# Kernel optimization log

Hardware: AMD Instinct MI355X
Metric: run time of the kernel (lower is better)

The kernel has to match this reference:

```python
import jax, jax.numpy as jnp
import numpy as np

B, D, H, L = 8, 512, 512, 8192


def _log_g(x):
    # log_g(x) = log(relu(x)+1) if x>=0 else x
    return jnp.where(x >= 0, jnp.log1p(jax.nn.relu(x)), x)


def setup_inputs() -> dict:
    key = jax.random.key(0)
    k1, k2, k3 = jax.random.split(key, 3)
    x = jax.random.normal(k1, (B, D, L), dtype=jnp.float32)
    # Conv1d(dim, 2*h_dim, kernel_size=1) weight [2H, D, 1] squeezed to [2H, D]
    W = jax.random.normal(k2, (2 * H, D), dtype=jnp.float32) / np.sqrt(D).astype(np.float32)
    b = jax.random.normal(k3, (2 * H,), dtype=jnp.float32) * 0.02
    return {"x": x, "W": W, "b": b}


def reference(x, W, b):
    # 1x1 conv == pointwise linear over channels: [B, 2H, L]
    hg = jnp.einsum('od,bdl->bol', W, x) + b[None, :, None]
    h, gate = jnp.split(hg, 2, axis=1)  # each [B, H, L]
    log_coeffs = -jax.nn.softplus(gate)                 # log(1 - sigmoid(gate))
    log_values = -jax.nn.softplus(-gate) + _log_g(h)    # log(sigmoid(gate)) + log_g(h)
    a_star = jnp.cumsum(log_coeffs, axis=2)
    log_h = a_star + jax.lax.cumlogsumexp(log_values - a_star, axis=2)
    return jnp.exp(log_h)  # [B, H, L]
```

## Files before the change

kernel.cpp:

```cpp
#include <hip/hip_runtime.h>
#include <hip/hip_fp16.h>

#define B_  8
#define D_  512
#define H_  512
#define L_  8192
#define O2_ 1024

typedef __attribute__((ext_vector_type(8))) short   bf16x8;
typedef __attribute__((ext_vector_type(4))) float   floatx4;
typedef __attribute__((ext_vector_type(8))) unsigned short ushort8_t;
typedef __attribute__((ext_vector_type(4))) unsigned short ushort4_t;

__device__ __forceinline__ unsigned short f2bf(float f) {
    union { float f; unsigned u; } x; x.f = f;
    unsigned u = x.u;
    u += 0x7FFFu + ((u >> 16) & 1u);
    return (unsigned short)(u >> 16);
}

__device__ __forceinline__ void async_load16(const void* g, void* l) {
    __builtin_amdgcn_global_load_lds(
        (const __attribute__((address_space(1))) unsigned int*)g,
        (__attribute__((address_space(3))) unsigned int*)l,
        16, 0, 0);
}

__global__ __launch_bounds__(256) void prep_w(const float* __restrict__ W,
                                              unsigned short* __restrict__ Wr) {
    int idx  = blockIdx.x * 256 + threadIdx.x;
    int flat = idx * 4;
    int o = flat >> 9;
    int d = flat & 511;
    int src_o = (o & 1) ? (H_ + (o >> 1)) : (o >> 1);
    float4 wv = *(const float4*)(W + (size_t)src_o * D_ + d);
    ushort4_t r;
    r.x = f2bf(wv.x); r.y = f2bf(wv.y); r.z = f2bf(wv.z); r.w = f2bf(wv.w);
    *(ushort4_t*)(Wr + (size_t)o * D_ + d) = r;
}

__global__ __launch_bounds__(256) void transpose_x(const float* __restrict__ x,
                                                   unsigned short* __restrict__ xT) {
    __shared__ float T[64][65];
    const int b  = blockIdx.z;
    const int d0 = blockIdx.y * 64;
    const int l0 = blockIdx.x * 64;
    const int tid = threadIdx.x;

    const int c  = tid & 15;
    const int r0 = tid >> 4;
    const float* xp = x + ((size_t)b * D_ + d0) * L_ + l0;
    for (int rr = r0; rr < 64; rr += 16) {
        float4 vv = *(const float4*)(xp + (size_t)rr * L_ + c * 4);
        T[c * 4 + 0][rr] = vv.x;
        T[c * 4 + 1][rr] = vv.y;
        T[c * 4 + 2][rr] = vv.z;
        T[c * 4 + 3][rr] = vv.w;
    }
    __syncthreads();

    const int dc  = (tid & 7) * 8;
    const int lr0 = tid >> 3;
    unsigned short* op = xT + ((size_t)b * L_ + l0) * D_ + d0;
    for (int lr = lr0; lr < 64; lr += 32) {
        ushort8_t o8;
        o8[0] = f2bf(T[lr][dc + 0]); o8[1] = f2bf(T[lr][dc + 1]);
        o8[2] = f2bf(T[lr][dc + 2]); o8[3] = f2bf(T[lr][dc + 3]);
        o8[4] = f2bf(T[lr][dc + 4]); o8[5] = f2bf(T[lr][dc + 5]);
        o8[6] = f2bf(T[lr][dc + 6]); o8[7] = f2bf(T[lr][dc + 7]);
        *(ushort8_t*)(op + (size_t)lr * D_ + dc) = o8;
    }
}

__global__ __launch_bounds__(256) void gemm_hg(const unsigned short* __restrict__ Wr,
                                               const unsigned short* __restrict__ xT,
                                               __half* __restrict__ hg) {
    __shared__ __align__(16) unsigned short As[128][64];
    __shared__ __align__(16) unsigned short Bs[128][64];

    const int b  = blockIdx.z;
    const int o0 = blockIdx.y * 128;
    const int l0 = blockIdx.x * 128;
    const int tid  = threadIdx.x;
    const int lane = tid & 63;
    const int w    = tid >> 6;
    const int wm   = (w >> 1) * 64;
    const int wn   = (w & 1) * 64;
    const int lm   = lane & 15;
    const int quad = lane >> 4;

    floatx4 acc[4][4];
    for (int mi = 0; mi < 4; ++mi)
        for (int ni = 0; ni < 4; ++ni)
            acc[mi][ni] = (floatx4){0.f, 0.f, 0.f, 0.f};

    const int srow = w * 32 + (lane >> 3);
    const int scol = (lane & 7) * 8;
    const unsigned short* Ag = Wr + (size_t)(o0 + srow) * D_ + scol;
    const unsigned short* Bg = xT + ((size_t)b * L_ + l0 + srow) * D_ + scol;

    for (int kk = 0; kk < 8; ++kk) {
        const int k0 = kk * 64;
        #pragma unroll
        for (int p = 0; p < 4; ++p) {
            async_load16(Ag + (size_t)(p * 8) * D_ + k0, &As[w * 32 + p * 8][0]);
            async_load16(Bg + (size_t)(p * 8) * D_ + k0, &Bs[w * 32 + p * 8][0]);
        }
        __syncthreads();

        #pragma unroll
        for (int ks = 0; ks < 2; ++ks) {
            const int koff = ks * 32 + quad * 8;
            bf16x8 af[4], bfv[4];
            #pragma unroll
            for (int mi = 0; mi < 4; ++mi)
                af[mi] = *(const bf16x8*)&As[wm + mi * 16 + lm][koff];
            #pragma unroll
            for (int ni = 0; ni < 4; ++ni)
                bfv[ni] = *(const bf16x8*)&Bs[wn + ni * 16 + lm][koff];
            #pragma unroll
            for (int mi = 0; mi < 4; ++mi)
                #pragma unroll
                for (int ni = 0; ni < 4; ++ni)
                    acc[mi][ni] = __builtin_amdgcn_mfma_f32_16x16x32_bf16(
                        af[mi], bfv[ni], acc[mi][ni], 0, 0, 0);
        }
        __syncthreads();
    }

    __half* hp = hg + ((size_t)b * O2_ + o0 + wm + quad * 4) * L_ + l0 + wn + lm;
    for (int mi = 0; mi < 4; ++mi)
        for (int ni = 0; ni < 4; ++ni)
            for (int r = 0; r < 4; ++r)
                hp[(size_t)(mi * 16 + r) * L_ + ni * 16] = __float2half(acc[mi][ni][r]);
}

__global__ __launch_bounds__(256, 3) void scan_seq(const __half* __restrict__ hg,
                                                   const float* __restrict__ bias,
                                                   float* __restrict__ out) {
    __shared__ __align__(16) unsigned int sBuf[256 * 40];
    __shared__ float sA[256];
    __shared__ float sB[256];
    unsigned int* sH = sBuf;
    unsigned int* sG = sBuf + 256 * 20;

    const int bid = blockIdx.x;
    const int b = bid >> 9;
    const int k = bid & 511;
    const int t = threadIdx.x;

    const uint4* hq = (const uint4*)(hg + ((size_t)b * O2_ + 2 * k) * L_);
    const uint4* gq = hq + (L_ / 8);

    #pragma unroll
    for (int j = 0; j < 4; ++j) {
        int idx = t + 256 * j;
        uint4 hv = hq[idx];
        uint4 gv = gq[idx];
        int cc = idx >> 2, ss = idx & 3;
        *(uint4*)&sH[cc * 20 + ss * 4] = hv;
        *(uint4*)&sG[cc * 20 + ss * 4] = gv;
    }
    const float bh = bias[k];
    const float bg = bias[H_ + k];
    __syncthreads();

    float c[32], v[32];
    float A = 1.f, Bv = 0.f;
    #pragma unroll
    for (int j4 = 0; j4 < 4; ++j4) {
        uint4 hv = *(const uint4*)&sH[t * 20 + j4 * 4];
        uint4 gv = *(const uint4*)&sG[t * 20 + j4 * 4];
        unsigned hu[4] = {hv.x, hv.y, hv.z, hv.w};
        unsigned gu[4] = {gv.x, gv.y, gv.z, gv.w};
        #pragma unroll
        for (int q = 0; q < 4; ++q) {
            __half2 h2 = *(const __half2*)&hu[q];
            __half2 g2 = *(const __half2*)&gu[q];
            #pragma unroll
            for (int e = 0; e < 2; ++e) {
                const int i = j4 * 8 + q * 2 + e;
                float hf = (e ? __high2float(h2) : __low2float(h2)) + bh;
                float gf = (e ? __high2float(g2) : __low2float(g2)) + bg;
                float ex  = __expf(gf);
                float inv = 1.f / (1.f + ex);
                float ci  = inv;
                float zi  = ex * inv;
                float gv2 = (hf >= 0.f) ? (1.f + hf) : __expf(hf);
                float vi  = zi * gv2;
                c[i] = ci; v[i] = vi;
                Bv = ci * Bv + vi;
                A *= ci;
            }
        }
    }

    sA[t] = A; sB[t] = Bv;
    __syncthreads();
    for (int off = 1; off < 256; off <<= 1) {
        float pA = 1.f, pB = 0.f;
        if (t >= off) { pA = sA[t - off]; pB = sB[t - off]; }
        __syncthreads();
        Bv = Bv + A * pB;
        A  = A * pA;
        sA[t] = A; sB[t] = Bv;
        __syncthreads();
    }
    float hr = (t > 0) ? sB[t - 1] : 0.f;

    float* sO = (float*)sBuf;
    #pragma unroll
    for (int i = 0; i < 32; i += 4) {
        float4 o4;
        o4.x = hr = c[i + 0] * hr + v[i + 0];
        o4.y = hr = c[i + 1] * hr + v[i + 1];
        o4.z = hr = c[i + 2] * hr + v[i + 2];
        o4.w = hr = c[i + 3] * hr + v[i + 3];
        *(float4*)&sO[t * 36 + i] = o4;
    }
    __syncthreads();

    float4* op4 = (float4*)(out + ((size_t)b * H_ + k) * L_);
    #pragma unroll
    for (int j = 0; j < 8; ++j) {
        int idx = t + 256 * j;
        int cc = idx >> 3, ss = idx & 7;
        op4[idx] = *(const float4*)&sO[cc * 36 + ss * 4];
    }
}

__global__ __launch_bounds__(256) void fused_naive(const float* __restrict__ x,
                                                   const float* __restrict__ W,
                                                   const float* __restrict__ bias,
                                                   float* __restrict__ out) {
    __shared__ float Wh[512];
    __shared__ float Wg[512];
    __shared__ float sA[256];
    __shared__ float sB[256];
    const int bid = blockIdx.x;
    const int b = bid >> 9;
    const int k = bid & 511;
    const int t = threadIdx.x;

    for (int i = t; i < 512; i += 256) {
        Wh[i] = W[(size_t)k * D_ + i];
        Wg[i] = W[(size_t)(H_ + k) * D_ + i];
    }
    const float bh = bias[k];
    const float bg = bias[H_ + k];
    __syncthreads();

    float Hc = 0.f;
    const float* xb = x + (size_t)b * D_ * L_;
    for (int ch = 0; ch < 32; ++ch) {
        const int l = ch * 256 + t;
        float ah = bh, ag = bg;
        for (int d = 0; d < 512; ++d) {
            float xv = xb[(size_t)d * L_ + l];
            ah += Wh[d] * xv;
            ag += Wg[d] * xv;
        }
        float e   = __expf(ag);
        float inv = 1.f / (1.f + e);
        float ci  = inv;
        float zi  = e * inv;
        float gv  = (ah >= 0.f) ? (1.f + ah) : __expf(ah);
        float vi  = zi * gv;

        float A = ci, Bv = vi;
        sA[t] = A; sB[t] = Bv;
        __syncthreads();
        for (int off = 1; off < 256; off <<= 1) {
            float pA = 1.f, pB = 0.f;
            if (t >= off) { pA = sA[t - off]; pB = sB[t - off]; }
            __syncthreads();
            Bv = Bv + A * pB;
            A  = A * pA;
            sA[t] = A; sB[t] = Bv;
            __syncthreads();
        }
        out[((size_t)b * H_ + k) * L_ + l] = A * Hc + Bv;
        float An = sA[255], Bn = sB[255];
        Hc = An * Hc + Bn;
        __syncthreads();
    }
}

extern "C" void kernel_launch(void* const* d_in, const int* in_sizes, int n_in,
                              void* d_out, int out_size, void* d_ws, size_t ws_size,
                              hipStream_t stream) {
    const float* x    = (const float*)d_in[0];
    const float* W    = (const float*)d_in[1];
    const float* bias = (const float*)d_in[2];
    float* out = (float*)d_out;

    const size_t xT_bytes = (size_t)B_ * L_ * D_ * 2;
    const size_t Wr_bytes = (size_t)O2_ * D_ * 2;
    const size_t hg_bytes = (size_t)B_ * O2_ * L_ * 2;
    const size_t need = xT_bytes + Wr_bytes + hg_bytes;

    if (ws_size >= need) {
        char* ws = (char*)d_ws;
        unsigned short* xT = (unsigned short*)ws;
        unsigned short* Wr = (unsigned short*)(ws + xT_bytes);
        __half*         hg = (__half*)(ws + xT_bytes + Wr_bytes);

        prep_w<<<512, 256, 0, stream>>>(W, Wr);
        transpose_x<<<dim3(L_ / 64, D_ / 64, B_), 256, 0, stream>>>(x, xT);
        gemm_hg<<<dim3(L_ / 128, O2_ / 128, B_), 256, 0, stream>>>(Wr, xT, hg);
        scan_seq<<<B_ * H_, 256, 0, stream>>>(hg, bias, out);
    } else {
        fused_naive<<<B_ * H_, 256, 0, stream>>>(x, W, bias, out);
    }
}
```

Baseline: 362.3 us.

## Swizzle GEMM LDS tiles and use wavefront-shuffle scan in scan kernel

The GEMM kernel now XOR-swizzles the 16-byte column groups of the A/B shared-memory tiles by row, on both the async global-to-LDS loads and the fragment reads, to cut LDS bank conflicts. In the scan kernel, the block-wide Hillis-Steele scan over shared memory, with two barriers per step, is replaced by an intra-wavefront shuffle scan plus a small cross-wave combine of four partials, leaving a single barrier. The min-blocks-per-SM launch bound on the scan kernel is also dropped, which may change register allocation and occupancy.

Result: faster. 345.2 us (-4.7%).

```diff
diff --git a/kernel.cpp b/kernel.cpp
--- a/kernel.cpp
+++ b/kernel.cpp
@@ -94,10 +94,10 @@
         for (int ni = 0; ni < 4; ++ni)
             acc[mi][ni] = (floatx4){0.f, 0.f, 0.f, 0.f};
 
-    const int srow = w * 32 + (lane >> 3);
-    const int scol = (lane & 7) * 8;
-    const unsigned short* Ag = Wr + (size_t)(o0 + srow) * D_ + scol;
-    const unsigned short* Bg = xT + ((size_t)b * L_ + l0 + srow) * D_ + scol;
+    const int sj  = lane >> 3;
+    const int scg = (lane & 7) ^ sj;
+    const unsigned short* Ag = Wr + (size_t)(o0 + w * 32 + sj) * D_ + scg * 8;
+    const unsigned short* Bg = xT + ((size_t)b * L_ + l0 + w * 32 + sj) * D_ + scg * 8;
 
     for (int kk = 0; kk < 8; ++kk) {
         const int k0 = kk * 64;
@@ -110,14 +110,18 @@
 
         #pragma unroll
         for (int ks = 0; ks < 2; ++ks) {
-            const int koff = ks * 32 + quad * 8;
+            const int lc = ks * 4 + quad;
             bf16x8 af[4], bfv[4];
             #pragma unroll
-            for (int mi = 0; mi < 4; ++mi)
-                af[mi] = *(const bf16x8*)&As[wm + mi * 16 + lm][koff];
+            for (int mi = 0; mi < 4; ++mi) {
+                const int r = wm + mi * 16 + lm;
+                af[mi] = *(const bf16x8*)&As[r][(lc ^ (r & 7)) * 8];
+            }
             #pragma unroll
-            for (int ni = 0; ni < 4; ++ni)
-                bfv[ni] = *(const bf16x8*)&Bs[wn + ni * 16 + lm][koff];
+            for (int ni = 0; ni < 4; ++ni) {
+                const int r = wn + ni * 16 + lm;
+                bfv[ni] = *(const bf16x8*)&Bs[r][(lc ^ (r & 7)) * 8];
+            }
             #pragma unroll
             for (int mi = 0; mi < 4; ++mi)
                 #pragma unroll
@@ -135,12 +139,12 @@
                 hp[(size_t)(mi * 16 + r) * L_ + ni * 16] = __float2half(acc[mi][ni][r]);
 }
 
-__global__ __launch_bounds__(256, 3) void scan_seq(const __half* __restrict__ hg,
-                                                   const float* __restrict__ bias,
-                                                   float* __restrict__ out) {
+__global__ __launch_bounds__(256) void scan_seq(const __half* __restrict__ hg,
+                                                const float* __restrict__ bias,
+                                                float* __restrict__ out) {
     __shared__ __align__(16) unsigned int sBuf[256 * 40];
-    __shared__ float sA[256];
-    __shared__ float sB[256];
+    __shared__ float wA[4];
+    __shared__ float wB[4];
     unsigned int* sH = sBuf;
     unsigned int* sG = sBuf + 256 * 20;
 
@@ -148,6 +152,8 @@
     const int b = bid >> 9;
     const int k = bid & 511;
     const int t = threadIdx.x;
+    const int lane = t & 63;
+    const int wid  = t >> 6;
 
     const uint4* hq = (const uint4*)(hg + ((size_t)b * O2_ + 2 * k) * L_);
     const uint4* gq = hq + (L_ / 8);
@@ -195,18 +201,23 @@
         }
     }
 
-    sA[t] = A; sB[t] = Bv;
-    __syncthreads();
-    for (int off = 1; off < 256; off <<= 1) {
-        float pA = 1.f, pB = 0.f;
-        if (t >= off) { pA = sA[t - off]; pB = sB[t - off]; }
-        __syncthreads();
-        Bv = Bv + A * pB;
-        A  = A * pA;
-        sA[t] = A; sB[t] = Bv;
-        __syncthreads();
-    }
-    float hr = (t > 0) ? sB[t - 1] : 0.f;
+    #pragma unroll
+    for (int off = 1; off < 64; off <<= 1) {
+        float pA = __shfl_up(A, off);
+        float pB = __shfl_up(Bv, off);
+        if (lane >= off) { Bv = Bv + A * pB; A = A * pA; }
+    }
+
+    if (lane == 63) { wA[wid] = A; wB[wid] = Bv; }
+    __syncthreads();
+
+    float cB = 0.f;
+    for (int p = 0; p < wid; ++p) cB = wB[p] + wA[p] * cB;
+
+    float eA = __shfl_up(A, 1);
+    float eB = __shfl_up(Bv, 1);
+    if (lane == 0) { eA = 1.f; eB = 0.f; }
+    float hr = eB + eA * cB;
 
     float* sO = (float*)sBuf;
     #pragma unroll
```
